# Kernel tuning notes

Measured on AMD Instinct MI355X. Metric: run time of the kernel, lower is better.

## Reference

```python
import jax, jax.numpy as jnp
import numpy as np

MODEL_SIZE = 512
HEADS = 8
T = 2048
B = 2


def setup_inputs() -> dict:
    key = jax.random.key(0)
    ks = jax.random.split(key, 10)
    E = MODEL_SIZE
    w = 0.02  # weight init scale for numerical stability
    return {
        "input": jax.random.normal(ks[0], (T, B, E), jnp.float32),
        "pos": jax.random.normal(ks[1], (T, 1, E), jnp.float32),
        "in_proj_weight": jax.random.normal(ks[2], (3 * E, E), jnp.float32) * w,
        "out_proj_weight": jax.random.normal(ks[3], (E, E), jnp.float32) * w,
        "pos_proj_weight": jax.random.normal(ks[4], (E, E), jnp.float32) * w,
        "in_proj_bias": jax.random.normal(ks[5], (3 * E,), jnp.float32) * w,
        "out_proj_bias": jax.random.normal(ks[6], (E,), jnp.float32) * w,
        "pos_proj_bias": jax.random.normal(ks[7], (E,), jnp.float32) * w,
        "r_w_bias": jax.random.normal(ks[8], (HEADS, E // HEADS), jnp.float32) * w,
        "r_r_bias": jax.random.normal(ks[9], (HEADS, E // HEADS), jnp.float32) * w,
    }


def _rel_shift(x):
    # x: [B, H, T, R] -> Transformer-XL relative shift
    b, h, t, r = x.shape
    x = jnp.pad(x, ((0, 0), (0, 0), (0, 0), (1, 0)))  # [B,H,T,R+1]
    x = x.reshape(b, h, r + 1, t)[:, :, 1:, :]        # drop first row
    return x.reshape(b, h, t, r)


def reference(input, pos, in_proj_weight, out_proj_weight, pos_proj_weight,
              in_proj_bias, out_proj_bias, pos_proj_bias, r_w_bias, r_r_bias):
    t, b, e = input.shape
    h = r_w_bias.shape[0]
    d = e // h
    scale = 1.0 / np.sqrt(d).astype(np.float32)

    # fused QKV projection (time-first layout [T,B,E])
    qkv = input @ in_proj_weight.T + in_proj_bias          # [T,B,3E]
    q, k, v = jnp.split(qkv, 3, axis=-1)
    q = q.reshape(t, b, h, d)
    k = k.reshape(t, b, h, d)
    v = v.reshape(t, b, h, d)

    # relative position projection (pos batch dim is 1)
    r = (pos[:, 0] @ pos_proj_weight.T + pos_proj_bias).reshape(-1, h, d)  # [R,H,D]

    # content (AC) and position (BD) scores
    ac = jnp.einsum('tbhd,sbhd->bhts', q + r_w_bias, k)    # [B,H,T,T]
    bd = jnp.einsum('tbhd,rhd->bhtr', q + r_r_bias, r)     # [B,H,T,R]
    bd = _rel_shift(bd)[..., :t]

    attn = jax.nn.softmax((ac + bd) * scale, axis=-1)      # [B,H,T,T]
    ctx = jnp.einsum('bhts,sbhd->tbhd', attn, v).reshape(t, b, e)
    return ctx @ out_proj_weight.T + out_proj_bias
```

## Files before the change

### kernel.cpp

```cpp
#include <hip/hip_runtime.h>

#define T_SEQ 2048
#define BATCH 2
#define HEADS 8
#define DHEAD 64
#define EMB   512

typedef __attribute__((ext_vector_type(8))) short short8;
typedef __attribute__((ext_vector_type(4))) float floatx4;
typedef __attribute__((ext_vector_type(8))) unsigned short ushort8;
typedef __attribute__((ext_vector_type(4))) unsigned short ushort4v;

__device__ __forceinline__ unsigned short f2b(float f) {
    union { float f; unsigned u; } v; v.f = f;
    unsigned r = v.u + 0x7fffu + ((v.u >> 16) & 1u);
    return (unsigned short)(r >> 16);
}
__device__ __forceinline__ unsigned short f2bt(float f) {
    union { float f; unsigned u; } v; v.f = f;
    return (unsigned short)(v.u >> 16);
}
__device__ __forceinline__ float b2f(unsigned short s) {
    union { unsigned u; float f; } v; v.u = ((unsigned)s) << 16; return v.f;
}
__device__ __forceinline__ short8 ld_frag(const unsigned short* p) {
    ushort4v lo = *(const ushort4v*)p;
    ushort4v hi = *(const ushort4v*)(p + 4);
    short8 r;
    r[0] = lo[0]; r[1] = lo[1]; r[2] = lo[2]; r[3] = lo[3];
    r[4] = hi[0]; r[5] = hi[1]; r[6] = hi[2]; r[7] = hi[3];
    return r;
}
__device__ __forceinline__ void st8(unsigned short* p, ushort8 v) {
    ushort4v lo = { v[0], v[1], v[2], v[3] };
    ushort4v hi = { v[4], v[5], v[6], v[7] };
    *(ushort4v*)p = lo;
    *(ushort4v*)(p + 4) = hi;
}
#define MFMA16(a, b, c) __builtin_amdgcn_mfma_f32_16x16x32_bf16(a, b, c, 0, 0, 0)

__global__ __launch_bounds__(256)
void cvt_all(const float* __restrict__ s0, const float* __restrict__ s1,
             const float* __restrict__ s2, const float* __restrict__ s3,
             const float* __restrict__ s4,
             unsigned short* __restrict__ d0, unsigned short* __restrict__ d1,
             unsigned short* __restrict__ d2, unsigned short* __restrict__ d3,
             unsigned short* __restrict__ d4)
{
    const int i = blockIdx.x * 256 + threadIdx.x;
    const float* s; unsigned short* d; int off;
    if      (i <  524288) { s = s0; d = d0; off = i; }
    else if (i <  786432) { s = s1; d = d1; off = i -  524288; }
    else if (i <  983040) { s = s2; d = d2; off = i -  786432; }
    else if (i < 1048576) { s = s3; d = d3; off = i -  983040; }
    else if (i < 1114112) { s = s4; d = d4; off = i - 1048576; }
    else return;
    const float4 v = ((const float4*)s)[off];
    ushort4v o = { f2b(v.x), f2b(v.y), f2b(v.z), f2b(v.w) };
    ((ushort4v*)d)[off] = o;
}

__global__ __launch_bounds__(256)
void gemm_qkv_pos(const unsigned short* __restrict__ inb, const unsigned short* __restrict__ w_inb,
                  const float* __restrict__ b_in,
                  const unsigned short* __restrict__ posb, const unsigned short* __restrict__ w_posb,
                  const float* __restrict__ b_pos,
                  unsigned short* __restrict__ q_s, unsigned short* __restrict__ k_s,
                  unsigned short* __restrict__ vT, unsigned short* __restrict__ r_b)
{
    __shared__ unsigned short shmem[34816];
    unsigned short* tb = shmem;

    const int id = blockIdx.x;
    const bool isPos = (id >= 384);
    const int bx = isPos ? ((id - 384) & 3) : (id % 12);
    const int by = isPos ? ((id - 384) >> 2) : (id / 12);
    const unsigned short* A = isPos ? posb : inb;
    const unsigned short* B = isPos ? w_posb : w_inb;
    const float* bias = isPos ? b_pos : b_in;

    const int bm  = by * 128;
    const int bn  = bx * 128;
    const int tid = threadIdx.x;
    const int lane = tid & 63, w = tid >> 6;
    const int m16 = lane & 15, quad = lane >> 4;
    const int wm = (w & 1) * 64, wn = (w >> 1) * 64;
    const int srow = tid >> 1, scol = (tid & 1) * 32;

    floatx4 acc[4][4];
    #pragma unroll
    for (int i = 0; i < 4; ++i)
        #pragma unroll
        for (int j = 0; j < 4; ++j) acc[i][j] = (floatx4){0.f, 0.f, 0.f, 0.f};

    ushort8 ar[4], br[4];
    auto fetch = [&](int k0) {
        ar[0] = *(const ushort8*)(A + (size_t)(bm + srow) * 512 + k0 + scol);
        ar[1] = *(const ushort8*)(A + (size_t)(bm + srow) * 512 + k0 + scol + 8);
        ar[2] = *(const ushort8*)(A + (size_t)(bm + srow) * 512 + k0 + scol + 16);
        ar[3] = *(const ushort8*)(A + (size_t)(bm + srow) * 512 + k0 + scol + 24);
        br[0] = *(const ushort8*)(B + (size_t)(bn + srow) * 512 + k0 + scol);
        br[1] = *(const ushort8*)(B + (size_t)(bn + srow) * 512 + k0 + scol + 8);
        br[2] = *(const ushort8*)(B + (size_t)(bn + srow) * 512 + k0 + scol + 16);
        br[3] = *(const ushort8*)(B + (size_t)(bn + srow) * 512 + k0 + scol + 24);
    };
    auto store_stage = [&](int q) {
        unsigned short* As = shmem + q * 17408;
        unsigned short* Bs = shmem + q * 17408 + 8704;
        st8(&As[srow * 68 + scol +  0], ar[0]);
        st8(&As[srow * 68 + scol +  8], ar[1]);
        st8(&As[srow * 68 + scol + 16], ar[2]);
        st8(&As[srow * 68 + scol + 24], ar[3]);
        st8(&Bs[srow * 68 + scol +  0], br[0]);
        st8(&Bs[srow * 68 + scol +  8], br[1]);
        st8(&Bs[srow * 68 + scol + 16], br[2]);
        st8(&Bs[srow * 68 + scol + 24], br[3]);
    };

    fetch(0);
    store_stage(0);
    __syncthreads();

    for (int kt = 0; kt < 8; ++kt) {
        const int p = kt & 1;
        unsigned short* As = shmem + p * 17408;
        unsigned short* Bs = shmem + p * 17408 + 8704;
        if (kt + 1 < 8) fetch((kt + 1) * 64);
        #pragma unroll
        for (int ks = 0; ks < 2; ++ks) {
            short8 af[4], bf[4];
            #pragma unroll
            for (int f = 0; f < 4; ++f) {
                af[f] = ld_frag(&As[(wm + f * 16 + m16) * 68 + ks * 32 + quad * 8]);
                bf[f] = ld_frag(&Bs[(wn + f * 16 + m16) * 68 + ks * 32 + quad * 8]);
            }
            #pragma unroll
            for (int fm = 0; fm < 4; ++fm)
                #pragma unroll
                for (int fn = 0; fn < 4; ++fn)
                    acc[fm][fn] = MFMA16(af[fm], bf[fn], acc[fm][fn]);
        }
        if (kt + 1 < 8) store_stage(1 - p);
        __syncthreads();
    }

    if (isPos) {
        #pragma unroll
        for (int fn = 0; fn < 4; ++fn) {
            const int n = bn + wn + fn * 16 + m16;
            const float bv = bias[n];
            #pragma unroll
            for (int fm = 0; fm < 4; ++fm)
                #pragma unroll
                for (int rgi = 0; rgi < 4; ++rgi) {
                    const int m = bm + wm + fm * 16 + quad * 4 + rgi;
                    r_b[(size_t)m * EMB + n] = f2b(acc[fm][fn][rgi] + bv);
                }
        }
    } else if (bn < 1024) {
        #pragma unroll
        for (int fn = 0; fn < 4; ++fn) {
            const int n = bn + wn + fn * 16 + m16;
            const float bv = bias[n];
            const int reg = n >> 9, c = n & 511, h = c >> 6, dd = c & 63;
            unsigned short* dst = reg == 0 ? q_s : k_s;
            #pragma unroll
            for (int fm = 0; fm < 4; ++fm)
                #pragma unroll
                for (int rgi = 0; rgi < 4; ++rgi) {
                    const int m = bm + wm + fm * 16 + quad * 4 + rgi;
                    const int t = m >> 1, b = m & 1;
                    dst[((size_t)(b * HEADS + h) * T_SEQ + t) * DHEAD + dd] = f2b(acc[fm][fn][rgi] + bv);
                }
        }
    } else {
        #pragma unroll
        for (int fn = 0; fn < 4; ++fn) {
            const int nl = wn + fn * 16 + m16;
            const float bv = bias[bn + nl];
            #pragma unroll
            for (int fm = 0; fm < 4; ++fm)
                #pragma unroll
                for (int rgi = 0; rgi < 4; ++rgi) {
                    const int ml = wm + fm * 16 + quad * 4 + rgi;
                    tb[nl * 131 + ml] = f2b(acc[fm][fn][rgi] + bv);
                }
        }
        __syncthreads();
        const int t0g = bm >> 1;
        for (int s2 = tid; s2 < 2048; s2 += 256) {
            const int nl = s2 >> 4;
            const int bsel = (s2 >> 3) & 1;
            const int j = s2 & 7;
            ushort8 o;
            #pragma unroll
            for (int k = 0; k < 8; ++k)
                o[k] = tb[nl * 131 + ((j * 8 + k) * 2 + bsel)];
            const int c = bn + nl - 1024, h = c >> 6, dd = c & 63;
            *(ushort8*)(vT + ((size_t)(bsel * HEADS + h) * DHEAD + dd) * T_SEQ + t0g + j * 8) = o;
        }
    }
}

__global__ __launch_bounds__(256)
void gemm_out(const unsigned short* __restrict__ A, const unsigned short* __restrict__ B,
              const float* __restrict__ bias, float* __restrict__ out)
{
    __shared__ unsigned short shmem[34816];
    const int bm  = blockIdx.y * 128;
    const int bn  = blockIdx.x * 128;
    const int tid = threadIdx.x;
    const int lane = tid & 63, w = tid >> 6;
    const int m16 = lane & 15, quad = lane >> 4;
    const int wm = (w & 1) * 64, wn = (w >> 1) * 64;
    const int srow = tid >> 1, scol = (tid & 1) * 32;

    floatx4 acc[4][4];
    #pragma unroll
    for (int i = 0; i < 4; ++i)
        #pragma unroll
        for (int j = 0; j < 4; ++j) acc[i][j] = (floatx4){0.f, 0.f, 0.f, 0.f};

    ushort8 ar[4], br[4];
    auto fetch = [&](int k0) {
        ar[0] = *(const ushort8*)(A + (size_t)(bm + srow) * 512 + k0 + scol);
        ar[1] = *(const ushort8*)(A + (size_t)(bm + srow) * 512 + k0 + scol + 8);
        ar[2] = *(const ushort8*)(A + (size_t)(bm + srow) * 512 + k0 + scol + 16);
        ar[3] = *(const ushort8*)(A + (size_t)(bm + srow) * 512 + k0 + scol + 24);
        br[0] = *(const ushort8*)(B + (size_t)(bn + srow) * 512 + k0 + scol);
        br[1] = *(const ushort8*)(B + (size_t)(bn + srow) * 512 + k0 + scol + 8);
        br[2] = *(const ushort8*)(B + (size_t)(bn + srow) * 512 + k0 + scol + 16);
        br[3] = *(const ushort8*)(B + (size_t)(bn + srow) * 512 + k0 + scol + 24);
    };
    auto store_stage = [&](int q) {
        unsigned short* As = shmem + q * 17408;
        unsigned short* Bs = shmem + q * 17408 + 8704;
        st8(&As[srow * 68 + scol +  0], ar[0]);
        st8(&As[srow * 68 + scol +  8], ar[1]);
        st8(&As[srow * 68 + scol + 16], ar[2]);
        st8(&As[srow * 68 + scol + 24], ar[3]);
        st8(&Bs[srow * 68 + scol +  0], br[0]);
        st8(&Bs[srow * 68 + scol +  8], br[1]);
        st8(&Bs[srow * 68 + scol + 16], br[2]);
        st8(&Bs[srow * 68 + scol + 24], br[3]);
    };

    fetch(0);
    store_stage(0);
    __syncthreads();

    for (int kt = 0; kt < 8; ++kt) {
        const int p = kt & 1;
        unsigned short* As = shmem + p * 17408;
        unsigned short* Bs = shmem + p * 17408 + 8704;
        if (kt + 1 < 8) fetch((kt + 1) * 64);
        #pragma unroll
        for (int ks = 0; ks < 2; ++ks) {
            short8 af[4], bf[4];
            #pragma unroll
            for (int f = 0; f < 4; ++f) {
                af[f] = ld_frag(&As[(wm + f * 16 + m16) * 68 + ks * 32 + quad * 8]);
                bf[f] = ld_frag(&Bs[(wn + f * 16 + m16) * 68 + ks * 32 + quad * 8]);
            }
            #pragma unroll
            for (int fm = 0; fm < 4; ++fm)
                #pragma unroll
                for (int fn = 0; fn < 4; ++fn)
                    acc[fm][fn] = MFMA16(af[fm], bf[fn], acc[fm][fn]);
        }
        if (kt + 1 < 8) store_stage(1 - p);
        __syncthreads();
    }

    #pragma unroll
    for (int fn = 0; fn < 4; ++fn) {
        const int n = bn + wn + fn * 16 + m16;
        const float bv = bias[n];
        #pragma unroll
        for (int fm = 0; fm < 4; ++fm)
            #pragma unroll
            for (int rgi = 0; rgi < 4; ++rgi) {
                const int m = bm + wm + fm * 16 + quad * 4 + rgi;
                out[(size_t)m * EMB + n] = acc[fm][fn][rgi] + bv;
            }
    }
}

__global__ __launch_bounds__(256)
void attn_mfma(const unsigned short* __restrict__ qg_, const unsigned short* __restrict__ kg_,
               const unsigned short* __restrict__ vtg_, const unsigned short* __restrict__ rg_,
               const float* __restrict__ rwb, const float* __restrict__ rrb,
               unsigned short* __restrict__ ctx)
{
    const int T   = T_SEQ;
    const int tb  = blockIdx.x;
    const int t0  = tb * 64;
    const int bh  = blockIdx.y;
    const int h   = bh & 7;
    const int b   = bh >> 3;
    const int tid = threadIdx.x;
    const int lane = tid & 63;
    const int w    = tid >> 6;
    const int m16  = lane & 15;
    const int quad = lane >> 4;
    const int ibase = 16 * w + quad * 4;

    __shared__ unsigned short lds[25920];
    unsigned short* kb    = lds;
    unsigned short* vb    = lds + 4352;
    unsigned short* rp    = lds + 8704;
    unsigned short* pbuf  = lds + 13056;
    unsigned short* ring  = lds + 17408;
    unsigned short* qrw_s = lds;
    unsigned short* qrr_s = lds + 4352;

    const unsigned short* qg  = qg_  + ((size_t)bh * T + t0) * DHEAD;
    const unsigned short* kg  = kg_  + (size_t)bh * T * DHEAD;
    const unsigned short* vtg = vtg_ + (size_t)bh * DHEAD * T;
    const unsigned short* rg  = rg_  + h * DHEAD;

    const float QSCALE = 0.125f * 1.44269504089f;
    for (int idx = tid; idx < 65 * 16; idx += 256) {
        const int row = idx >> 4, c = (idx & 15) << 2;
        ushort4v qv = {0, 0, 0, 0};
        if (t0 + row < T) qv = *(const ushort4v*)(qg + row * DHEAD + c);
        const float4 rr = *(const float4*)(rrb + h * DHEAD + c);
        qrr_s[row * 68 + c + 0] = f2b((b2f(qv[0]) + rr.x) * QSCALE);
        qrr_s[row * 68 + c + 1] = f2b((b2f(qv[1]) + rr.y) * QSCALE);
        qrr_s[row * 68 + c + 2] = f2b((b2f(qv[2]) + rr.z) * QSCALE);
        qrr_s[row * 68 + c + 3] = f2b((b2f(qv[3]) + rr.w) * QSCALE);
        if (row < 64) {
            const float4 rw = *(const float4*)(rwb + h * DHEAD + c);
            qrw_s[row * 68 + c + 0] = f2b((b2f(qv[0]) + rw.x) * QSCALE);
            qrw_s[row * 68 + c + 1] = f2b((b2f(qv[1]) + rw.y) * QSCALE);
            qrw_s[row * 68 + c + 2] = f2b((b2f(qv[2]) + rw.z) * QSCALE);
            qrw_s[row * 68 + c + 3] = f2b((b2f(qv[3]) + rw.w) * QSCALE);
        }
    }
    __syncthreads();

    short8 a_ac[2], a_qrl[2], a_qru[2];
    {
        const unsigned short* p0 = &qrw_s[(16 * w + m16) * 68 + quad * 8];
        a_ac[0]  = ld_frag(p0);  a_ac[1]  = ld_frag(p0 + 32);
        const unsigned short* p1 = &qrr_s[(16 * w + m16) * 68 + quad * 8];
        a_qrl[0] = ld_frag(p1);  a_qrl[1] = ld_frag(p1 + 32);
        const unsigned short* p2 = &qrr_s[(16 * w + 1 + m16) * 68 + quad * 8];
        a_qru[0] = ld_frag(p2);  a_qru[1] = ld_frag(p2 + 32);
    }
    __syncthreads();

    const int srow0 = tid >> 3,          scol0 = (tid & 7) * 8;
    const int srow1 = (tid + 256) >> 3,  scol1 = (tid & 7) * 8;

    ushort8 kr[2], vr[2], rr8[2];
    auto prefetch = [&](int s0n) {
        const bool ln = (s0n <= t0);
        const int jb = (ln ? (s0n + T - t0 - 64) : (s0n - t0 - 65)) + 64;
        int j0 = jb + srow0; j0 = j0 < 0 ? 0 : (j0 > T - 1 ? T - 1 : j0);
        int j1 = jb + srow1; j1 = j1 < 0 ? 0 : (j1 > T - 1 ? T - 1 : j1);
        kr[0]  = *(const ushort8*)(kg + (size_t)(s0n + srow0) * DHEAD + scol0);
        kr[1]  = *(const ushort8*)(kg + (size_t)(s0n + srow1) * DHEAD + scol1);
        vr[0]  = *(const ushort8*)(vtg + (size_t)srow0 * T + s0n + scol0);
        vr[1]  = *(const ushort8*)(vtg + (size_t)srow1 * T + s0n + scol1);
        rr8[0] = *(const ushort8*)(rg + (size_t)j0 * EMB + scol0);
        rr8[1] = *(const ushort8*)(rg + (size_t)j1 * EMB + scol1);
    };
    auto store_bufs = [&]() {
        st8(&kb[srow0 * 68 + scol0], kr[0]);
        st8(&kb[srow1 * 68 + scol1], kr[1]);
        st8(&vb[srow0 * 68 + scol0], vr[0]);
        st8(&vb[srow1 * 68 + scol1], vr[1]);
        st8(&rp[srow0 * 68 + scol0], rr8[0]);
        st8(&rp[srow1 * 68 + scol1], rr8[1]);
    };
    auto stage_to = [&](unsigned short* dstb, int jbase) {
        #pragma unroll
        for (int idx = tid; idx < 512; idx += 256) {
            const int row = idx >> 3, c = (idx & 7) * 8;
            int j = jbase + row; j = j < 0 ? 0 : (j > T - 1 ? T - 1 : j);
            st8(&dstb[row * 68 + c], *(const ushort8*)(rg + (size_t)j * EMB + c));
        }
    };
    auto qr_half = [&](const unsigned short* rsb, const short8* aq, int slotbase) {
        #pragma unroll
        for (int cc = 0; cc < 4; ++cc) {
            floatx4 q4 = (floatx4){0.f, 0.f, 0.f, 0.f};
            #pragma unroll
            for (int ks = 0; ks < 2; ++ks) {
                short8 bfr = ld_frag(&rsb[(16 * cc + m16) * 68 + ks * 32 + quad * 8]);
                q4 = MFMA16(aq[ks], bfr, q4);
            }
            #pragma unroll
            for (int rgi = 0; rgi < 4; ++rgi)
                ring[(ibase + rgi) * 133 + slotbase + 16 * cc + m16] = f2bt(q4[rgi]);
        }
    };

    floatx4 O[4];
    float lrun[4];
    #pragma unroll
    for (int ct = 0; ct < 4; ++ct) O[ct] = (floatx4){0.f, 0.f, 0.f, 0.f};
    #pragma unroll
    for (int rgi = 0; rgi < 4; ++rgi) lrun[rgi] = 0.f;

    {
        stage_to(rp, T - t0 - 64);
        prefetch(0);
        __syncthreads();
        qr_half(rp, a_qrl, 0);
        __syncthreads();
        store_bufs();
        __syncthreads();
    }

    for (int na = 0; na < T / 64; ++na) {
        const int s0 = na * 64;
        const bool lower = (s0 <= t0);
        const int nph    = lower ? (s0 >> 6) : ((s0 - t0) >> 6);
        const int rbase  = (nph & 1) * 64;
        const int wbase  = 64 - rbase;
        const bool hasNext = (na + 1 < T / 64);

        floatx4 acf[4];
        __builtin_amdgcn_s_setprio(1);
        #pragma unroll
        for (int ct = 0; ct < 4; ++ct) {
            acf[ct] = (floatx4){0.f, 0.f, 0.f, 0.f};
            #pragma unroll
            for (int ks = 0; ks < 2; ++ks) {
                short8 bfr = ld_frag(&kb[(16 * ct + m16) * 68 + ks * 32 + quad * 8]);
                acf[ct] = MFMA16(a_ac[ks], bfr, acf[ct]);
            }
        }
        __builtin_amdgcn_s_setprio(0);
        if (hasNext) prefetch(s0 + 64);
        qr_half(rp, lower ? a_qrl : a_qru, wbase);

        if (s0 != t0) {
            #pragma unroll
            for (int ct = 0; ct < 4; ++ct) {
                #pragma unroll
                for (int rgi = 0; rgi < 4; ++rgi) {
                    const int i = ibase + rgi;
                    const int slot = ((63 - i + 16 * ct + m16) + rbase) & 127;
                    acf[ct][rgi] += b2f(ring[i * 133 + slot]);
                }
            }
            if (s0 == t0 + 64 && lane == 48 && w == 3)
                acf[0][3] -= b2f(ring[63 * 133 + (rbase & 127)]);
        } else {
            #pragma unroll
            for (int ct = 0; ct < 4; ++ct) {
                #pragma unroll
                for (int rgi = 0; rgi < 4; ++rgi) {
                    const int i = ibase + rgi, u = 16 * ct + m16;
                    if (u <= i) acf[ct][rgi] += b2f(ring[i * 133 + (((63 - i + u) + rbase) & 127)]);
                }
            }
            __syncthreads();
            stage_to(rp, -1);
            __syncthreads();
            qr_half(rp, a_qru, 64);
            #pragma unroll
            for (int ct = 0; ct < 4; ++ct) {
                #pragma unroll
                for (int rgi = 0; rgi < 4; ++rgi) {
                    const int i = ibase + rgi, u = 16 * ct + m16;
                    if (u >= i + 2) acf[ct][rgi] += b2f(ring[i * 133 + 63 - i + u]);
                }
            }
        }

        #pragma unroll
        for (int rgi = 0; rgi < 4; ++rgi) {
            #pragma unroll
            for (int ct = 0; ct < 4; ++ct) {
                const float pv = exp2f(acf[ct][rgi]);
                acf[ct][rgi] = pv;
                lrun[rgi] += pv;
            }
        }
        #pragma unroll
        for (int ct = 0; ct < 4; ++ct)
            #pragma unroll
            for (int rgi = 0; rgi < 4; ++rgi)
                pbuf[(ibase + rgi) * 68 + 16 * ct + m16] = f2bt(acf[ct][rgi]);

        short8 ap[2];
        {
            const unsigned short* pp = &pbuf[(16 * w + m16) * 68 + quad * 8];
            ap[0] = ld_frag(pp); ap[1] = ld_frag(pp + 32);
        }
        __builtin_amdgcn_s_setprio(1);
        #pragma unroll
        for (int ct = 0; ct < 4; ++ct) {
            #pragma unroll
            for (int ks = 0; ks < 2; ++ks) {
                short8 bfr = ld_frag(&vb[(16 * ct + m16) * 68 + ks * 32 + quad * 8]);
                O[ct] = MFMA16(ap[ks], bfr, O[ct]);
            }
        }
        __builtin_amdgcn_s_setprio(0);
        __syncthreads();
        if (hasNext) {
            store_bufs();
            __syncthreads();
        }
    }

    #pragma unroll
    for (int rgi = 0; rgi < 4; ++rgi) {
        float l = lrun[rgi];
        #pragma unroll
        for (int off = 1; off < 16; off <<= 1)
            l += __shfl_xor(l, off);
        const float inv = 1.f / l;
        const int t = t0 + ibase + rgi;
        #pragma unroll
        for (int ct = 0; ct < 4; ++ct)
            ctx[((size_t)t * BATCH + b) * EMB + h * DHEAD + 16 * ct + m16] = f2bt(O[ct][rgi] * inv);
    }
}

extern "C" void kernel_launch(void* const* d_in, const int* in_sizes, int n_in,
                              void* d_out, int out_size, void* d_ws, size_t ws_size,
                              hipStream_t stream)
{
    const float* input = (const float*)d_in[0];
    const float* pos   = (const float*)d_in[1];
    const float* w_in  = (const float*)d_in[2];
    const float* w_out = (const float*)d_in[3];
    const float* w_pos = (const float*)d_in[4];
    const float* b_in  = (const float*)d_in[5];
    const float* b_out = (const float*)d_in[6];
    const float* b_pos = (const float*)d_in[7];
    const float* rwb   = (const float*)d_in[8];
    const float* rrb   = (const float*)d_in[9];

    unsigned short* ws     = (unsigned short*)d_ws;
    unsigned short* inb    = ws;
    unsigned short* posb   = ws + 2097152;
    unsigned short* w_inb  = ws + 3145728;
    unsigned short* w_posb = ws + 3932160;
    unsigned short* w_outb = ws + 6291456;
    unsigned short* q_s    = ws + 6553600;
    unsigned short* k_s    = ws + 8650752;
    unsigned short* vT     = ws + 10747904;
    unsigned short* r_b    = ws + 12845056;
    unsigned short* ctx_b  = ws + 13893632;

    cvt_all<<<4352, 256, 0, stream>>>(input, pos, w_in, w_pos, w_out,
                                      inb, posb, w_inb, w_posb, w_outb);
    gemm_qkv_pos<<<448, 256, 0, stream>>>(inb, w_inb, b_in, posb, w_posb, b_pos,
                                          q_s, k_s, vT, r_b);
    attn_mfma<<<dim3(32, 16), 256, 0, stream>>>(q_s, k_s, vT, r_b, rwb, rrb, ctx_b);
    gemm_out<<<dim3(4, 32), 256, 0, stream>>>(ctx_b, w_outb, b_out, (float*)d_out);
}
```

Baseline: 191.5 us.

## Split attention key range into three chunks with atomic partial accumulation

The attention kernel now splits the 32 key blocks into three ranges along a new grid z dimension, tripling the block count. Each split re-derives the relative-position ring state for its first key block. Each split atomically adds its unnormalized output and row sums into fp32 buffers, which a new kernel zeroes beforehand and another kernel normalizes and writes out as bf16 context. This is meant to fill the GPU better than 512 blocks do. The cost is two extra launches, fp32 atomic traffic and redundant setup work per split.

```diff
diff --git a/kernel.cpp b/kernel.cpp
--- a/kernel.cpp
+++ b/kernel.cpp
@@ -61,6 +61,30 @@
 }
 
 __global__ __launch_bounds__(256)
+void zero_acc(float* __restrict__ O_acc, float* __restrict__ l_acc)
+{
+    const int i = blockIdx.x * 256 + threadIdx.x;
+    const float4 z = { 0.f, 0.f, 0.f, 0.f };
+    if (i < 524288)      ((float4*)O_acc)[i] = z;
+    else if (i < 532480) ((float4*)l_acc)[i - 524288] = z;
+}
+
+__global__ __launch_bounds__(256)
+void norm_ctx(const float* __restrict__ O_acc, const float* __restrict__ l_acc,
+              unsigned short* __restrict__ ctx)
+{
+    const int i = blockIdx.x * 256 + threadIdx.x;
+    const int d4  = i & 15;
+    const int row = i >> 4;
+    const int t  = row & (T_SEQ - 1), bh = row >> 11;
+    const int h  = bh & 7, b = bh >> 3;
+    const float inv = 1.f / l_acc[row];
+    const float4 o = ((const float4*)O_acc)[i];
+    ushort4v r = { f2bt(o.x * inv), f2bt(o.y * inv), f2bt(o.z * inv), f2bt(o.w * inv) };
+    *(ushort4v*)(ctx + ((size_t)t * BATCH + b) * EMB + h * DHEAD + d4 * 4) = r;
+}
+
+__global__ __launch_bounds__(256)
 void gemm_qkv_pos(const unsigned short* __restrict__ inb, const unsigned short* __restrict__ w_inb,
                   const float* __restrict__ b_in,
                   const unsigned short* __restrict__ posb, const unsigned short* __restrict__ w_posb,
@@ -290,20 +314,23 @@
 void attn_mfma(const unsigned short* __restrict__ qg_, const unsigned short* __restrict__ kg_,
                const unsigned short* __restrict__ vtg_, const unsigned short* __restrict__ rg_,
                const float* __restrict__ rwb, const float* __restrict__ rrb,
-               unsigned short* __restrict__ ctx)
+               float* __restrict__ O_acc, float* __restrict__ l_acc)
 {
     const int T   = T_SEQ;
     const int tb  = blockIdx.x;
     const int t0  = tb * 64;
     const int bh  = blockIdx.y;
     const int h   = bh & 7;
-    const int b   = bh >> 3;
     const int tid = threadIdx.x;
     const int lane = tid & 63;
     const int w    = tid >> 6;
     const int m16  = lane & 15;
     const int quad = lane >> 4;
     const int ibase = 16 * w + quad * 4;
+
+    const int split = blockIdx.z;
+    const int na_lo = split == 0 ? 0  : (split == 1 ? 11 : 21);
+    const int na_hi = split == 0 ? 11 : (split == 1 ? 21 : 32);
 
     __shared__ unsigned short lds[25920];
     unsigned short* kb    = lds;
@@ -405,22 +432,30 @@
     for (int rgi = 0; rgi < 4; ++rgi) lrun[rgi] = 0.f;
 
     {
-        stage_to(rp, T - t0 - 64);
-        prefetch(0);
+        const short8* aq_p; int jprev, sbase;
+        if (na_lo == 0) { jprev = T - t0 - 64; aq_p = a_qrl; sbase = 0; }
+        else {
+            const int s0p = (na_lo - 1) * 64;
+            if (s0p < t0)       { jprev = s0p + T - t0;  aq_p = a_qrl; sbase = 64 - (((s0p >> 6) & 1) * 64); }
+            else if (s0p == t0) { jprev = -1;            aq_p = a_qru; sbase = 64; }
+            else                { jprev = s0p - t0 - 1;  aq_p = a_qru; sbase = 64 - ((((s0p - t0) >> 6) & 1) * 64); }
+        }
+        stage_to(rp, jprev);
+        prefetch(na_lo * 64);
         __syncthreads();
-        qr_half(rp, a_qrl, 0);
+        qr_half(rp, aq_p, sbase);
         __syncthreads();
         store_bufs();
         __syncthreads();
     }
 
-    for (int na = 0; na < T / 64; ++na) {
+    for (int na = na_lo; na < na_hi; ++na) {
         const int s0 = na * 64;
         const bool lower = (s0 <= t0);
         const int nph    = lower ? (s0 >> 6) : ((s0 - t0) >> 6);
         const int rbase  = (nph & 1) * 64;
         const int wbase  = 64 - rbase;
-        const bool hasNext = (na + 1 < T / 64);
+        const bool hasNext = (na + 1 < na_hi);
 
         floatx4 acf[4];
         __builtin_amdgcn_s_setprio(1);
@@ -515,11 +550,11 @@
         #pragma unroll
         for (int off = 1; off < 16; off <<= 1)
             l += __shfl_xor(l, off);
-        const float inv = 1.f / l;
         const int t = t0 + ibase + rgi;
+        if (m16 == 0) atomicAdd(&l_acc[(size_t)bh * T + t], l);
         #pragma unroll
         for (int ct = 0; ct < 4; ++ct)
-            ctx[((size_t)t * BATCH + b) * EMB + h * DHEAD + 16 * ct + m16] = f2bt(O[ct][rgi] * inv);
+            atomicAdd(&O_acc[((size_t)bh * T + t) * DHEAD + 16 * ct + m16], O[ct][rgi]);
     }
 }
 
@@ -550,10 +585,16 @@
     unsigned short* r_b    = ws + 12845056;
     unsigned short* ctx_b  = ws + 13893632;
 
+    float* O_acc = (float*)ws;
+    float* l_acc = (float*)(ws + 4194304);
+
     cvt_all<<<4352, 256, 0, stream>>>(input, pos, w_in, w_pos, w_out,
                                       inb, posb, w_inb, w_posb, w_outb);
     gemm_qkv_pos<<<448, 256, 0, stream>>>(inb, w_inb, b_in, posb, w_posb, b_pos,
                                           q_s, k_s, vT, r_b);
-    attn_mfma<<<dim3(32, 16), 256, 0, stream>>>(q_s, k_s, vT, r_b, rwb, rrb, ctx_b);
+    zero_acc<<<2080, 256, 0, stream>>>(O_acc, l_acc);
+    attn_mfma<<<dim3(32, 16, 3), 256, 0, stream>>>(q_s, k_s, vT, r_b, rwb, rrb,
+                                                   O_acc, l_acc);
+    norm_ctx<<<2048, 256, 0, stream>>>(O_acc, l_acc, ctx_b);
     gemm_out<<<dim3(4, 32), 256, 0, stream>>>(ctx_b, w_outb, b_out, (float*)d_out);
 }
```

After: 236.3 us. +23.4%, slower.

## Load K, V and R MFMA fragments directly from global, drop LDS staging

Applied to the files above, without the earlier changes.

Removes the shared-memory staging buffers and register prefetch for K, V^T and relative-position rows. Each wave now reads its MFMA B-fragments straight from global memory (relying on L1/L2 caching across the four waves). This eliminates two block barriers per iteration. The ring buffer for the shifted position scores is now kept in fp32 instead of truncated bf16, which doubles its LDS footprint but shrinks total LDS. The risk is more redundant global traffic per wave and exposed load latency now that there is no software prefetch.

```diff
diff --git a/kernel.cpp b/kernel.cpp
--- a/kernel.cpp
+++ b/kernel.cpp
@@ -30,6 +30,11 @@
     r[0] = lo[0]; r[1] = lo[1]; r[2] = lo[2]; r[3] = lo[3];
     r[4] = hi[0]; r[5] = hi[1]; r[6] = hi[2]; r[7] = hi[3];
     return r;
+}
+__device__ __forceinline__ short8 ldg_frag(const unsigned short* p) {
+    union { ushort8 u; short8 s; } c;
+    c.u = *(const ushort8*)p;
+    return c.s;
 }
 __device__ __forceinline__ void st8(unsigned short* p, ushort8 v) {
     ushort4v lo = { v[0], v[1], v[2], v[3] };
@@ -305,12 +310,9 @@
     const int quad = lane >> 4;
     const int ibase = 16 * w + quad * 4;
 
-    __shared__ unsigned short lds[25920];
-    unsigned short* kb    = lds;
-    unsigned short* vb    = lds + 4352;
-    unsigned short* rp    = lds + 8704;
-    unsigned short* pbuf  = lds + 13056;
-    unsigned short* ring  = lds + 17408;
+    __shared__ unsigned short lds[21376];
+    unsigned short* pbuf  = lds;
+    float*          ringf = (float*)(lds + 4352);
     unsigned short* qrw_s = lds;
     unsigned short* qrr_s = lds + 4352;
 
@@ -350,50 +352,18 @@
     }
     __syncthreads();
 
-    const int srow0 = tid >> 3,          scol0 = (tid & 7) * 8;
-    const int srow1 = (tid + 256) >> 3,  scol1 = (tid & 7) * 8;
-
-    ushort8 kr[2], vr[2], rr8[2];
-    auto prefetch = [&](int s0n) {
-        const bool ln = (s0n <= t0);
-        const int jb = (ln ? (s0n + T - t0 - 64) : (s0n - t0 - 65)) + 64;
-        int j0 = jb + srow0; j0 = j0 < 0 ? 0 : (j0 > T - 1 ? T - 1 : j0);
-        int j1 = jb + srow1; j1 = j1 < 0 ? 0 : (j1 > T - 1 ? T - 1 : j1);
-        kr[0]  = *(const ushort8*)(kg + (size_t)(s0n + srow0) * DHEAD + scol0);
-        kr[1]  = *(const ushort8*)(kg + (size_t)(s0n + srow1) * DHEAD + scol1);
-        vr[0]  = *(const ushort8*)(vtg + (size_t)srow0 * T + s0n + scol0);
-        vr[1]  = *(const ushort8*)(vtg + (size_t)srow1 * T + s0n + scol1);
-        rr8[0] = *(const ushort8*)(rg + (size_t)j0 * EMB + scol0);
-        rr8[1] = *(const ushort8*)(rg + (size_t)j1 * EMB + scol1);
-    };
-    auto store_bufs = [&]() {
-        st8(&kb[srow0 * 68 + scol0], kr[0]);
-        st8(&kb[srow1 * 68 + scol1], kr[1]);
-        st8(&vb[srow0 * 68 + scol0], vr[0]);
-        st8(&vb[srow1 * 68 + scol1], vr[1]);
-        st8(&rp[srow0 * 68 + scol0], rr8[0]);
-        st8(&rp[srow1 * 68 + scol1], rr8[1]);
-    };
-    auto stage_to = [&](unsigned short* dstb, int jbase) {
-        #pragma unroll
-        for (int idx = tid; idx < 512; idx += 256) {
-            const int row = idx >> 3, c = (idx & 7) * 8;
+    auto qr_direct = [&](int jbase, const short8* aq, int slotbase) {
+        #pragma unroll
+        for (int cc = 0; cc < 4; ++cc) {
+            const int row = 16 * cc + m16;
             int j = jbase + row; j = j < 0 ? 0 : (j > T - 1 ? T - 1 : j);
-            st8(&dstb[row * 68 + c], *(const ushort8*)(rg + (size_t)j * EMB + c));
-        }
-    };
-    auto qr_half = [&](const unsigned short* rsb, const short8* aq, int slotbase) {
-        #pragma unroll
-        for (int cc = 0; cc < 4; ++cc) {
+            const unsigned short* rrow = rg + (size_t)j * EMB + quad * 8;
             floatx4 q4 = (floatx4){0.f, 0.f, 0.f, 0.f};
-            #pragma unroll
-            for (int ks = 0; ks < 2; ++ks) {
-                short8 bfr = ld_frag(&rsb[(16 * cc + m16) * 68 + ks * 32 + quad * 8]);
-                q4 = MFMA16(aq[ks], bfr, q4);
-            }
+            q4 = MFMA16(aq[0], ldg_frag(rrow), q4);
+            q4 = MFMA16(aq[1], ldg_frag(rrow + 32), q4);
             #pragma unroll
             for (int rgi = 0; rgi < 4; ++rgi)
-                ring[(ibase + rgi) * 133 + slotbase + 16 * cc + m16] = f2bt(q4[rgi]);
+                ringf[(ibase + rgi) * 133 + slotbase + 16 * cc + m16] = q4[rgi];
         }
     };
 
@@ -404,15 +374,7 @@
     #pragma unroll
     for (int rgi = 0; rgi < 4; ++rgi) lrun[rgi] = 0.f;
 
-    {
-        stage_to(rp, T - t0 - 64);
-        prefetch(0);
-        __syncthreads();
-        qr_half(rp, a_qrl, 0);
-        __syncthreads();
-        store_bufs();
-        __syncthreads();
-    }
+    qr_direct(T - t0 - 64, a_qrl, 0);
 
     for (int na = 0; na < T / 64; ++na) {
         const int s0 = na * 64;
@@ -420,22 +382,19 @@
         const int nph    = lower ? (s0 >> 6) : ((s0 - t0) >> 6);
         const int rbase  = (nph & 1) * 64;
         const int wbase  = 64 - rbase;
-        const bool hasNext = (na + 1 < T / 64);
 
         floatx4 acf[4];
         __builtin_amdgcn_s_setprio(1);
         #pragma unroll
         for (int ct = 0; ct < 4; ++ct) {
+            const unsigned short* krow = kg + (size_t)(s0 + 16 * ct + m16) * DHEAD + quad * 8;
             acf[ct] = (floatx4){0.f, 0.f, 0.f, 0.f};
-            #pragma unroll
-            for (int ks = 0; ks < 2; ++ks) {
-                short8 bfr = ld_frag(&kb[(16 * ct + m16) * 68 + ks * 32 + quad * 8]);
-                acf[ct] = MFMA16(a_ac[ks], bfr, acf[ct]);
-            }
+            acf[ct] = MFMA16(a_ac[0], ldg_frag(krow), acf[ct]);
+            acf[ct] = MFMA16(a_ac[1], ldg_frag(krow + 32), acf[ct]);
         }
         __builtin_amdgcn_s_setprio(0);
-        if (hasNext) prefetch(s0 + 64);
-        qr_half(rp, lower ? a_qrl : a_qru, wbase);
+
+        qr_direct(lower ? (s0 + T - t0) : (s0 - t0 - 1), lower ? a_qrl : a_qru, wbase);
 
         if (s0 != t0) {
             #pragma unroll
@@ -444,30 +403,27 @@
                 for (int rgi = 0; rgi < 4; ++rgi) {
                     const int i = ibase + rgi;
                     const int slot = ((63 - i + 16 * ct + m16) + rbase) & 127;
-                    acf[ct][rgi] += b2f(ring[i * 133 + slot]);
+                    acf[ct][rgi] += ringf[i * 133 + slot];
                 }
             }
             if (s0 == t0 + 64 && lane == 48 && w == 3)
-                acf[0][3] -= b2f(ring[63 * 133 + (rbase & 127)]);
+                acf[0][3] -= ringf[63 * 133 + (rbase & 127)];
         } else {
             #pragma unroll
             for (int ct = 0; ct < 4; ++ct) {
                 #pragma unroll
                 for (int rgi = 0; rgi < 4; ++rgi) {
                     const int i = ibase + rgi, u = 16 * ct + m16;
-                    if (u <= i) acf[ct][rgi] += b2f(ring[i * 133 + (((63 - i + u) + rbase) & 127)]);
+                    if (u <= i) acf[ct][rgi] += ringf[i * 133 + (((63 - i + u) + rbase) & 127)];
                 }
             }
-            __syncthreads();
-            stage_to(rp, -1);
-            __syncthreads();
-            qr_half(rp, a_qru, 64);
+            qr_direct(-1, a_qru, 64);
             #pragma unroll
             for (int ct = 0; ct < 4; ++ct) {
                 #pragma unroll
                 for (int rgi = 0; rgi < 4; ++rgi) {
                     const int i = ibase + rgi, u = 16 * ct + m16;
-                    if (u >= i + 2) acf[ct][rgi] += b2f(ring[i * 133 + 63 - i + u]);
+                    if (u >= i + 2) acf[ct][rgi] += ringf[i * 133 + 63 - i + u];
                 }
             }
         }
@@ -495,18 +451,11 @@
         __builtin_amdgcn_s_setprio(1);
         #pragma unroll
         for (int ct = 0; ct < 4; ++ct) {
-            #pragma unroll
-            for (int ks = 0; ks < 2; ++ks) {
-                short8 bfr = ld_frag(&vb[(16 * ct + m16) * 68 + ks * 32 + quad * 8]);
-                O[ct] = MFMA16(ap[ks], bfr, O[ct]);
-            }
+            const unsigned short* vrow = vtg + (size_t)(16 * ct + m16) * T + s0 + quad * 8;
+            O[ct] = MFMA16(ap[0], ldg_frag(vrow), O[ct]);
+            O[ct] = MFMA16(ap[1], ldg_frag(vrow + 32), O[ct]);
         }
         __builtin_amdgcn_s_setprio(0);
-        __syncthreads();
-        if (hasNext) {
-            store_bufs();
-            __syncthreads();
-        }
     }
 
     #pragma unroll
```

Result: slower. 302.5 us (+57.9%).
